# Optimization experiments

Measured on AMD Instinct MI355X. Metric: run time of the kernel, lower is better.

Reference implementation:

```python
import jax, jax.numpy as jnp
import numpy as np

B, D, E, H = 2048, 1024, 16, 4096
NUM_ACTIVE = 2
LN_EPS = 1e-5
NORM_EPS = 1e-12


def setup_inputs() -> dict:
    key = jax.random.key(0)
    ks = jax.random.split(key, 4)
    s1 = 1.0 / np.sqrt(D)
    s2 = 1.0 / np.sqrt(H)
    return {
        "input": jax.random.normal(ks[0], (B, D), jnp.float32),
        "ln_gamma": jnp.ones((D,), jnp.float32),
        "ln_beta": jnp.zeros((D,), jnp.float32),
        "expert_keys": jax.random.normal(ks[1], (D, E), jnp.float32),
        "W1": jax.random.normal(ks[2], (E, D, H), jnp.float32) * s1,
        "b1": jnp.zeros((E, H), jnp.float32),
        "W2": jax.random.normal(ks[3], (E, H, D), jnp.float32) * s2,
        "b2": jnp.zeros((E, D), jnp.float32),
    }


def reference(input, ln_gamma, ln_beta, expert_keys, W1, b1, W2, b2):
    # Gating: LayerNorm(input) @ normalize(expert_keys, dim=-1)
    mu = jnp.mean(input, axis=-1, keepdims=True)
    var = jnp.mean((input - mu) ** 2, axis=-1, keepdims=True)
    xn = (input - mu) / jnp.sqrt(var + LN_EPS) * ln_gamma + ln_beta
    # F.normalize(expert_keys, dim=-1): each row (per feature) normalized over experts
    keys = expert_keys / jnp.clip(
        jnp.linalg.norm(expert_keys, axis=-1, keepdims=True), NORM_EPS)
    logits = xn @ keys  # [B, E]
    # Top-k routing (argsort descending, take first num_active)
    top_vals, top_ids = jax.lax.top_k(logits, NUM_ACTIVE)  # [B, k]
    gates_k = jax.nn.softmax(top_vals, axis=-1)            # softmax over chosen logits
    gates = jnp.zeros_like(logits).at[
        jnp.arange(logits.shape[0])[:, None], top_ids].set(gates_k)  # [B, E]
    # Experts applied to RAW input (not the normalized gating input), dense-all-experts
    h = jax.nn.relu(jnp.einsum('bd,edh->beh', input, W1) + b1)   # [B, E, H]
    eo = jnp.einsum('beh,ehd->bed', h, W2) + b2                  # [B, E, D]
    # Weighted combine: only top-k experts have nonzero gates
    out = jnp.einsum('bed,be->bd', eo, gates)                    # [B, D]
    return out
```

## Files before the change

### kernel.cpp

```cpp
#include <hip/hip_runtime.h>
#include <hip/hip_bf16.h>
#include <cstdint>
#include <cstddef>

#define D_ 1024
#define H_ 4096
#define E_ 16
#define B_ 2048

constexpr int CAP = 384;

typedef __attribute__((ext_vector_type(4))) float f32x4;
typedef __attribute__((ext_vector_type(8))) short bf16x8;

__device__ __forceinline__ unsigned pack2(float a, float b) {
  __hip_bfloat162 h = __float22bfloat162_rn(make_float2(a, b));
  union { __hip_bfloat162 h2; unsigned u; } cv; cv.h2 = h;
  return cv.u;
}
__device__ __forceinline__ float bflo(unsigned u) { return __uint_as_float(u << 16); }
__device__ __forceinline__ float bfhi(unsigned u) { return __uint_as_float(u & 0xffff0000u); }

#define GLL16(g, l)                                                         \
  __builtin_amdgcn_global_load_lds(                                         \
      (const __attribute__((address_space(1))) void*)(g),                   \
      (__attribute__((address_space(3))) void*)(l), 16, 0, 0)

#define WAITV(n) asm volatile("s_waitcnt vmcnt(" #n ")" ::: "memory")
#define WAITL()  asm volatile("s_waitcnt lgkmcnt(0)" ::: "memory")
#define MEMBAR() asm volatile("" ::: "memory")
#define BAR() __builtin_amdgcn_s_barrier()

__global__ void moe_zero(int* __restrict__ cnt) {
  if (threadIdx.x < E_) cnt[threadIdx.x] = 0;
}

__global__ __launch_bounds__(256) void moe_gating3(
    const float* __restrict__ x, const float* __restrict__ gamma,
    const float* __restrict__ beta, const float* __restrict__ keys,
    int* __restrict__ cnt, int4* __restrict__ rmi, float2* __restrict__ rmg,
    unsigned short* __restrict__ xg)
{
  const int b = blockIdx.x, t = threadIdx.x;
  const int w = t >> 6;
  const float4 xv = ((const float4*)(x + (size_t)b * D_))[t];
  float s  = xv.x + xv.y + xv.z + xv.w;
  float sq = xv.x*xv.x + xv.y*xv.y + xv.z*xv.z + xv.w*xv.w;
#pragma unroll
  for (int off = 32; off >= 1; off >>= 1) {
    s  += __shfl_down(s, off);
    sq += __shfl_down(sq, off);
  }
  __shared__ float ssum[4], ssq[4], sstat[2];
  if ((t & 63) == 0) { ssum[w] = s; ssq[w] = sq; }
  __syncthreads();
  if (t == 0) {
    float S = ssum[0] + ssum[1] + ssum[2] + ssum[3];
    float Q = ssq[0] + ssq[1] + ssq[2] + ssq[3];
    float mu  = S * (1.0f / D_);
    float var = Q * (1.0f / D_) - mu * mu;
    sstat[0] = mu; sstat[1] = rsqrtf(var + 1e-5f);
  }
  __syncthreads();
  const float mu = sstat[0], rstd = sstat[1];
  const float4 gv = ((const float4*)gamma)[t];
  const float4 bv = ((const float4*)beta)[t];
  float xn[4] = {(xv.x-mu)*rstd*gv.x+bv.x, (xv.y-mu)*rstd*gv.y+bv.y,
                 (xv.z-mu)*rstd*gv.z+bv.z, (xv.w-mu)*rstd*gv.w+bv.w};
  float acc[E_];
#pragma unroll
  for (int e2 = 0; e2 < E_; ++e2) acc[e2] = 0.f;
#pragma unroll
  for (int j = 0; j < 4; ++j) {
    const int d = 4*t + j;
    const float* kr = keys + (size_t)d * E_;
    float kv[E_];
#pragma unroll
    for (int e2 = 0; e2 < E_; ++e2) kv[e2] = kr[e2];
    float nq = 0.f;
#pragma unroll
    for (int e2 = 0; e2 < E_; ++e2) nq += kv[e2] * kv[e2];
    const float sc = xn[j] / fmaxf(sqrtf(nq), 1e-12f);
#pragma unroll
    for (int e2 = 0; e2 < E_; ++e2) acc[e2] += sc * kv[e2];
  }
#pragma unroll
  for (int off = 1; off < 64; off <<= 1) {
#pragma unroll
    for (int e2 = 0; e2 < E_; ++e2) acc[e2] += __shfl_xor(acc[e2], off);
  }
  __shared__ float wred[4][E_];
  if ((t & 63) == 0) {
#pragma unroll
    for (int e2 = 0; e2 < E_; ++e2) wred[w][e2] = acc[e2];
  }
  __syncthreads();
  __shared__ int sE[2], sP[2];
  if (t == 0) {
    float lg[E_];
#pragma unroll
    for (int e2 = 0; e2 < E_; ++e2)
      lg[e2] = wred[0][e2] + wred[1][e2] + wred[2][e2] + wred[3][e2];
    float v0 = -1e30f; int e0 = 0;
    for (int e2 = 0; e2 < E_; ++e2) { if (lg[e2] > v0) { v0 = lg[e2]; e0 = e2; } }
    float v1 = -1e30f; int e1 = 0;
    for (int e2 = 0; e2 < E_; ++e2) { if (e2 == e0) continue; if (lg[e2] > v1) { v1 = lg[e2]; e1 = e2; } }
    const float g0 = 1.f / (1.f + __expf(v1 - v0));
    const float g1 = 1.f - g0;
    int p0 = atomicAdd(cnt + e0, 1); if (p0 >= CAP) p0 = CAP - 1;
    int p1 = atomicAdd(cnt + e1, 1); if (p1 >= CAP) p1 = CAP - 1;
    rmi[b] = make_int4(e0, p0, e1, p1);
    rmg[b] = make_float2(g0, g1);
    sE[0] = e0; sP[0] = p0;
    sE[1] = e1; sP[1] = p1;
  }
  __syncthreads();
  const uint2 pk = make_uint2(pack2(xv.x, xv.y), pack2(xv.z, xv.w));
#pragma unroll
  for (int i = 0; i < 2; ++i)
    ((uint2*)(xg + ((size_t)sE[i] * CAP + sP[i]) * D_))[t] = pk;
}

template<int KROW, int KLEN, int WN, int SPLITK, bool RELU>
__global__ void __launch_bounds__(256, 3)
moe_gemm(const unsigned short* __restrict__ Asrc, const float* __restrict__ W,
         const float* __restrict__ bias, const int* __restrict__ cnt,
         unsigned short* __restrict__ d0, unsigned short* __restrict__ d1,
         unsigned short* __restrict__ d2, unsigned short* __restrict__ d3)
{
  constexpr int NPHASE = KLEN / 32;
  constexpr int NT = WN / 128;
  constexpr int MT = 3;

  const int bx = blockIdx.x;
  const int xcd = bx & 7;
  int slot = bx >> 3;
  const int mt = slot % MT; slot /= MT;
  const int nt = slot % NT; slot /= NT;
  const int eh = slot & 1;  slot >>= 1;
  const int part = slot;
  const int e  = (xcd << 1) | eh;
  const int nb = nt * 128;
  const int koff = part * KLEN;
  unsigned short* dst = (part == 0) ? d0 : (part == 1) ? d1 : (part == 2) ? d2 : d3;

  int cntE = cnt[e]; if (cntE > CAP) cntE = CAP;
  if (mt * 128 >= cntE) return;

  const int t = threadIdx.x, w = t >> 6, lane = t & 63;
  const int l15 = lane & 15, l4 = lane >> 4;

  __shared__ __align__(16) unsigned short As[2][128 * 32];
  __shared__ __align__(16) unsigned short Bs[2][128 * 32];

  asm volatile("s_waitcnt vmcnt(0) lgkmcnt(0)" ::: "memory");

  const unsigned short* Ae = Asrc + (size_t)e * CAP * KROW + (size_t)mt * 128 * KROW + koff;
  const float* We = W + (size_t)e * KROW * WN + (size_t)koff * WN + nb;

  const unsigned short *srcA0, *srcA1;
  {
    const int c0 = t,        r0 = c0 >> 2;
    const int c1 = t + 256,  r1 = c1 >> 2;
    srcA0 = Ae + (size_t)r0 * KROW + ((c0 & 3) ^ ((r0 >> 1) & 3)) * 8;
    srcA1 = Ae + (size_t)r1 * KROW + ((c1 & 3) ^ ((r1 >> 1) & 3)) * 8;
  }
  const int bn = t & 127, bkh = t >> 7;
  const float* srcB = We + (size_t)(bkh * 16) * WN + bn;
  const int bo0 = bn * 64 + (((bkh * 2 + 0) ^ ((bn >> 1) & 3)) << 4);
  const int bo1 = bn * 64 + (((bkh * 2 + 1) ^ ((bn >> 1) & 3)) << 4);

  float R0[16], R1[16];

#define ISSUE_A(p, BUF) do {                                                \
    const int ko_ = (p) * 32;                                               \
    GLL16(srcA0 + ko_, &As[BUF][(0 * 256 + w * 64) * 8]);                   \
    GLL16(srcA1 + ko_, &As[BUF][(1 * 256 + w * 64) * 8]);                   \
  } while (0)

#define ISSUE_B(p, Rv) do {                                                 \
    const float* bp_ = srcB + (size_t)(p) * 32 * WN;                        \
    _Pragma("unroll")                                                       \
    for (int j = 0; j < 16; ++j)                                            \
      Rv[j] = bp_[(size_t)j * WN];                                          \
  } while (0)

#define WRITE(Rv, BUF) do {                                                 \
    uint4 q0_, q1_;                                                         \
    q0_.x = pack2(Rv[0],  Rv[1]);  q0_.y = pack2(Rv[2],  Rv[3]);            \
    q0_.z = pack2(Rv[4],  Rv[5]);  q0_.w = pack2(Rv[6],  Rv[7]);            \
    q1_.x = pack2(Rv[8],  Rv[9]);  q1_.y = pack2(Rv[10], Rv[11]);           \
    q1_.z = pack2(Rv[12], Rv[13]); q1_.w = pack2(Rv[14], Rv[15]);           \
    *(uint4*)((char*)&Bs[BUF][0] + bo0) = q0_;                              \
    *(uint4*)((char*)&Bs[BUF][0] + bo1) = q1_;                              \
  } while (0)

  f32x4 acc[8][2];
#pragma unroll
  for (int rf = 0; rf < 8; ++rf) { acc[rf][0] = f32x4{0,0,0,0}; acc[rf][1] = f32x4{0,0,0,0}; }

  const int swA = (l15 >> 1) & 3;
  const int mrow0 = mt * 128;

#define COMP(BUF) do {                                                      \
    bf16x8 BB[2];                                                           \
    _Pragma("unroll")                                                       \
    for (int cf = 0; cf < 2; ++cf) {                                        \
      const int n_ = w * 32 + cf * 16 + l15;                                \
      BB[cf] = *(const bf16x8*)((const char*)&Bs[BUF][0]                    \
               + (n_ * 64 + ((l4 ^ ((n_ >> 1) & 3)) << 4)));                \
    }                                                                       \
    __builtin_amdgcn_s_setprio(1);                                          \
    _Pragma("unroll")                                                       \
    for (int rf = 0; rf < 8; ++rf) {                                        \
      if (mrow0 + rf * 16 < cntE) {                                         \
        const bf16x8 a = *(const bf16x8*)&As[BUF][((rf * 16 + l15) * 4 + (l4 ^ swA)) * 8]; \
        acc[rf][0] = __builtin_amdgcn_mfma_f32_16x16x32_bf16(a, BB[0], acc[rf][0], 0,0,0); \
        acc[rf][1] = __builtin_amdgcn_mfma_f32_16x16x32_bf16(a, BB[1], acc[rf][1], 0,0,0); \
      }                                                                     \
    }                                                                       \
    __builtin_amdgcn_s_setprio(0);                                          \
  } while (0)

  ISSUE_A(0, 0); MEMBAR();
  ISSUE_B(0, R0); MEMBAR();
  ISSUE_B(1, R1);
#pragma unroll 1
  for (int p = 0; p < NPHASE; p += 2) {
    if (p + 1 < NPHASE) { WAITV(16); } else { WAITV(0); }
    WRITE(R0, 0);
    if (p + 1 < NPHASE) { ISSUE_A(p + 1, 1); }
    MEMBAR();
    if (p + 2 < NPHASE) { ISSUE_B(p + 2, R0); }
    WAITL(); BAR();
    COMP(0);
    BAR();
    if (p + 1 < NPHASE) {
      if (p + 2 < NPHASE) { WAITV(16); } else { WAITV(0); }
      WRITE(R1, 1);
      if (p + 2 < NPHASE) { ISSUE_A(p + 2, 0); }
      MEMBAR();
      if (p + 3 < NPHASE) { ISSUE_B(p + 3, R1); }
      WAITL(); BAR();
      COMP(1);
      BAR();
    }
  }
#undef ISSUE_A
#undef ISSUE_B
#undef WRITE
#undef COMP

  unsigned short* dbase = dst + (size_t)e * CAP * WN + nb + w * 32;
#pragma unroll
  for (int rf = 0; rf < 8; ++rf) {
    if (mrow0 + rf * 16 >= cntE && rf > 0) continue;
#pragma unroll
    for (int cf = 0; cf < 2; ++cf) {
      float bv = 0.f;
      if constexpr (RELU) bv = bias[e * WN + nb + w * 32 + cf * 16 + l15];
#pragma unroll
      for (int r = 0; r < 4; ++r) {
        const int row = mrow0 + rf * 16 + l4 * 4 + r;
        float v = acc[rf][cf][r];
        if constexpr (RELU) v = fmaxf(v + bv, 0.f);
        const unsigned u01 = pack2(v, __shfl_xor(v, 1));
        const float uo = __shfl_xor(__uint_as_float(u01), 2);
        if ((l15 & 3) == 0)
          *(uint2*)(dbase + (size_t)row * WN + cf * 16 + l15) =
              make_uint2(u01, __float_as_uint(uo));
      }
    }
  }
}

__global__ __launch_bounds__(256) void moe_comb(
    const unsigned short* __restrict__ p0, const unsigned short* __restrict__ p1,
    const unsigned short* __restrict__ p2, const unsigned short* __restrict__ p3,
    const float* __restrict__ b2, const int4* __restrict__ rmi,
    const float2* __restrict__ rmg, float* __restrict__ out)
{
  const int b = blockIdx.x, t = threadIdx.x;
  const int4 m = rmi[b];
  const float2 g = rmg[b];
  const int c = t * 4;
  const size_t offA = ((size_t)m.x * CAP + m.y) * D_ + c;
  const size_t offB = ((size_t)m.z * CAP + m.w) * D_ + c;
  float a0, a1, a2, a3, c0, c1, c2, c3;
  {
    const uint2 ua = *(const uint2*)(p0 + offA);
    const uint2 ub = *(const uint2*)(p0 + offB);
    a0 = bflo(ua.x); a1 = bfhi(ua.x); a2 = bflo(ua.y); a3 = bfhi(ua.y);
    c0 = bflo(ub.x); c1 = bfhi(ub.x); c2 = bflo(ub.y); c3 = bfhi(ub.y);
  }
  const unsigned short* parts[3] = { p1, p2, p3 };
#pragma unroll
  for (int i = 0; i < 3; ++i) {
    if (parts[i] != nullptr) {
      const uint2 ua = *(const uint2*)(parts[i] + offA);
      const uint2 ub = *(const uint2*)(parts[i] + offB);
      a0 += bflo(ua.x); a1 += bfhi(ua.x); a2 += bflo(ua.y); a3 += bfhi(ua.y);
      c0 += bflo(ub.x); c1 += bfhi(ub.x); c2 += bflo(ub.y); c3 += bfhi(ub.y);
    }
  }
  const float4 b2a = *(const float4*)(b2 + (size_t)m.x * D_ + c);
  const float4 b2b = *(const float4*)(b2 + (size_t)m.z * D_ + c);
  float4 o;
  o.x = g.x * (a0 + b2a.x) + g.y * (c0 + b2b.x);
  o.y = g.x * (a1 + b2a.y) + g.y * (c1 + b2b.y);
  o.z = g.x * (a2 + b2a.z) + g.y * (c2 + b2b.z);
  o.w = g.x * (a3 + b2a.w) + g.y * (c3 + b2b.w);
  *(float4*)(out + (size_t)b * D_ + c) = o;
}

extern "C" void kernel_launch(void* const* d_in, const int* in_sizes, int n_in,
                              void* d_out, int out_size, void* d_ws, size_t ws_size,
                              hipStream_t stream) {
  const float* x     = (const float*)d_in[0];
  const float* gamma = (const float*)d_in[1];
  const float* beta  = (const float*)d_in[2];
  const float* keys  = (const float*)d_in[3];
  const float* W1    = (const float*)d_in[4];
  const float* b1    = (const float*)d_in[5];
  const float* W2    = (const float*)d_in[6];
  const float* b2    = (const float*)d_in[7];
  float* out = (float*)d_out;

  char* ws = (char*)d_ws;
  const size_t OFF_RMI = 256;
  const size_t OFF_RMG = OFF_RMI + (size_t)B_ * 16;
  const size_t OFF_XG  = OFF_RMG + (size_t)B_ * 8;
  const size_t EO_SZ   = (size_t)E_ * CAP * D_ * 2;
  const size_t OFF_HW  = OFF_XG + EO_SZ;
  const size_t HW_SZ   = (size_t)E_ * CAP * H_ * 2;
  const size_t OFF_EO1 = OFF_HW + HW_SZ;
  const size_t NEED2   = OFF_EO1 + EO_SZ;
  const size_t NEED4   = OFF_EO1 + 3 * EO_SZ;

  int*    cnt = (int*)ws;
  int4*   rmi = (int4*)(ws + OFF_RMI);
  float2* rmg = (float2*)(ws + OFF_RMG);
  unsigned short* xg  = (unsigned short*)(ws + OFF_XG);
  unsigned short* eo0 = xg;
  unsigned short* hws = (unsigned short*)(ws + OFF_HW);

  moe_zero<<<1, 64, 0, stream>>>(cnt);
  moe_gating3<<<B_, 256, 0, stream>>>(x, gamma, beta, keys, cnt, rmi, rmg, xg);

  moe_gemm<D_, D_, H_, 1, true><<<1536, 256, 0, stream>>>(
      xg, W1, b1, cnt, hws, nullptr, nullptr, nullptr);

  if (ws_size >= NEED4) {
    unsigned short* eo1 = (unsigned short*)(ws + OFF_EO1);
    unsigned short* eo2 = (unsigned short*)(ws + OFF_EO1 + EO_SZ);
    unsigned short* eo3 = (unsigned short*)(ws + OFF_EO1 + 2 * EO_SZ);
    moe_gemm<H_, H_ / 4, D_, 4, false><<<1536, 256, 0, stream>>>(
        hws, W2, nullptr, cnt, eo0, eo1, eo2, eo3);
    moe_comb<<<B_, 256, 0, stream>>>(eo0, eo1, eo2, eo3, b2, rmi, rmg, out);
  } else if (ws_size >= NEED2) {
    unsigned short* eo1 = (unsigned short*)(ws + OFF_EO1);
    moe_gemm<H_, H_ / 2, D_, 2, false><<<768, 256, 0, stream>>>(
        hws, W2, nullptr, cnt, eo0, eo1, nullptr, nullptr);
    moe_comb<<<B_, 256, 0, stream>>>(eo0, eo1, nullptr, nullptr, b2, rmi, rmg, out);
  } else {
    moe_gemm<H_, H_, D_, 1, false><<<384, 256, 0, stream>>>(
        hws, W2, nullptr, cnt, eo0, nullptr, nullptr, nullptr);
    moe_comb<<<B_, 256, 0, stream>>>(eo0, nullptr, nullptr, nullptr, b2, rmi, rmg, out);
  }
}
```

Measured before the change: 297.0 us.

## Enlarge MoE GEMM tiles to 256 rows with 512-thread blocks and capacity 512

The grouped expert GEMM now uses 256x128 tiles computed by 8 waves, each owning 32 rows by all 128 columns, instead of 128x128 tiles split by column. Each fp32 weight tile converted to bf16 is therefore reused across twice as many token rows, which cuts the repeated weight loads and conversions. Expert capacity rises from 384 to 512, and the grid is re-decomposed into two M-tiles per expert. The costs are more padded work for experts with fewer tokens, more LDS per block and lower occupancy, and larger workspace buffers.

```diff
diff --git a/kernel.cpp b/kernel.cpp
--- a/kernel.cpp
+++ b/kernel.cpp
@@ -8,7 +8,7 @@
 #define E_ 16
 #define B_ 2048
 
-constexpr int CAP = 384;
+constexpr int CAP = 512;
 
 typedef __attribute__((ext_vector_type(4))) float f32x4;
 typedef __attribute__((ext_vector_type(8))) short bf16x8;
@@ -122,7 +122,7 @@
 }
 
 template<int KROW, int KLEN, int WN, int SPLITK, bool RELU>
-__global__ void __launch_bounds__(256, 3)
+__global__ void __launch_bounds__(512, 2)
 moe_gemm(const unsigned short* __restrict__ Asrc, const float* __restrict__ W,
          const float* __restrict__ bias, const int* __restrict__ cnt,
          unsigned short* __restrict__ d0, unsigned short* __restrict__ d1,
@@ -130,12 +130,11 @@
 {
   constexpr int NPHASE = KLEN / 32;
   constexpr int NT = WN / 128;
-  constexpr int MT = 3;
 
   const int bx = blockIdx.x;
   const int xcd = bx & 7;
   int slot = bx >> 3;
-  const int mt = slot % MT; slot /= MT;
+  const int mt = slot & 1;  slot >>= 1;
   const int nt = slot % NT; slot /= NT;
   const int eh = slot & 1;  slot >>= 1;
   const int part = slot;
@@ -145,78 +144,75 @@
   unsigned short* dst = (part == 0) ? d0 : (part == 1) ? d1 : (part == 2) ? d2 : d3;
 
   int cntE = cnt[e]; if (cntE > CAP) cntE = CAP;
-  if (mt * 128 >= cntE) return;
+  if (mt * 256 >= cntE) return;
 
   const int t = threadIdx.x, w = t >> 6, lane = t & 63;
   const int l15 = lane & 15, l4 = lane >> 4;
 
-  __shared__ __align__(16) unsigned short As[2][128 * 32];
+  __shared__ __align__(16) unsigned short As[2][256 * 32];
   __shared__ __align__(16) unsigned short Bs[2][128 * 32];
 
   asm volatile("s_waitcnt vmcnt(0) lgkmcnt(0)" ::: "memory");
 
-  const unsigned short* Ae = Asrc + (size_t)e * CAP * KROW + (size_t)mt * 128 * KROW + koff;
+  const unsigned short* Ae = Asrc + (size_t)e * CAP * KROW + (size_t)mt * 256 * KROW + koff;
   const float* We = W + (size_t)e * KROW * WN + (size_t)koff * WN + nb;
 
   const unsigned short *srcA0, *srcA1;
   {
     const int c0 = t,        r0 = c0 >> 2;
-    const int c1 = t + 256,  r1 = c1 >> 2;
+    const int c1 = t + 512,  r1 = c1 >> 2;
     srcA0 = Ae + (size_t)r0 * KROW + ((c0 & 3) ^ ((r0 >> 1) & 3)) * 8;
     srcA1 = Ae + (size_t)r1 * KROW + ((c1 & 3) ^ ((r1 >> 1) & 3)) * 8;
   }
-  const int bn = t & 127, bkh = t >> 7;
-  const float* srcB = We + (size_t)(bkh * 16) * WN + bn;
-  const int bo0 = bn * 64 + (((bkh * 2 + 0) ^ ((bn >> 1) & 3)) << 4);
-  const int bo1 = bn * 64 + (((bkh * 2 + 1) ^ ((bn >> 1) & 3)) << 4);
-
-  float R0[16], R1[16];
+  const int bn = t & 127, bkq = t >> 7;
+  const float* srcB = We + (size_t)(bkq * 8) * WN + bn;
+  const int bo = bn * 64 + ((bkq ^ ((bn >> 1) & 3)) << 4);
+
+  float R0[8], R1[8];
 
 #define ISSUE_A(p, BUF) do {                                                \
     const int ko_ = (p) * 32;                                               \
-    GLL16(srcA0 + ko_, &As[BUF][(0 * 256 + w * 64) * 8]);                   \
-    GLL16(srcA1 + ko_, &As[BUF][(1 * 256 + w * 64) * 8]);                   \
+    GLL16(srcA0 + ko_, &As[BUF][(0 * 512 + w * 64) * 8]);                   \
+    GLL16(srcA1 + ko_, &As[BUF][(1 * 512 + w * 64) * 8]);                   \
   } while (0)
 
 #define ISSUE_B(p, Rv) do {                                                 \
     const float* bp_ = srcB + (size_t)(p) * 32 * WN;                        \
     _Pragma("unroll")                                                       \
-    for (int j = 0; j < 16; ++j)                                            \
+    for (int j = 0; j < 8; ++j)                                             \
       Rv[j] = bp_[(size_t)j * WN];                                          \
   } while (0)
 
 #define WRITE(Rv, BUF) do {                                                 \
-    uint4 q0_, q1_;                                                         \
-    q0_.x = pack2(Rv[0],  Rv[1]);  q0_.y = pack2(Rv[2],  Rv[3]);            \
-    q0_.z = pack2(Rv[4],  Rv[5]);  q0_.w = pack2(Rv[6],  Rv[7]);            \
-    q1_.x = pack2(Rv[8],  Rv[9]);  q1_.y = pack2(Rv[10], Rv[11]);           \
-    q1_.z = pack2(Rv[12], Rv[13]); q1_.w = pack2(Rv[14], Rv[15]);           \
-    *(uint4*)((char*)&Bs[BUF][0] + bo0) = q0_;                              \
-    *(uint4*)((char*)&Bs[BUF][0] + bo1) = q1_;                              \
+    uint4 q_;                                                               \
+    q_.x = pack2(Rv[0], Rv[1]);  q_.y = pack2(Rv[2], Rv[3]);                \
+    q_.z = pack2(Rv[4], Rv[5]);  q_.w = pack2(Rv[6], Rv[7]);                \
+    *(uint4*)((char*)&Bs[BUF][0] + bo) = q_;                                \
   } while (0)
 
-  f32x4 acc[8][2];
-#pragma unroll
-  for (int rf = 0; rf < 8; ++rf) { acc[rf][0] = f32x4{0,0,0,0}; acc[rf][1] = f32x4{0,0,0,0}; }
+  f32x4 acc[2][8];
+#pragma unroll
+  for (int rf = 0; rf < 2; ++rf)
+#pragma unroll
+    for (int cf = 0; cf < 8; ++cf) acc[rf][cf] = f32x4{0,0,0,0};
 
   const int swA = (l15 >> 1) & 3;
-  const int mrow0 = mt * 128;
+  const int mrow0 = mt * 256;
+  const int wrow = w * 32;
 
 #define COMP(BUF) do {                                                      \
-    bf16x8 BB[2];                                                           \
-    _Pragma("unroll")                                                       \
-    for (int cf = 0; cf < 2; ++cf) {                                        \
-      const int n_ = w * 32 + cf * 16 + l15;                                \
-      BB[cf] = *(const bf16x8*)((const char*)&Bs[BUF][0]                    \
-               + (n_ * 64 + ((l4 ^ ((n_ >> 1) & 3)) << 4)));                \
-    }                                                                       \
     __builtin_amdgcn_s_setprio(1);                                          \
     _Pragma("unroll")                                                       \
-    for (int rf = 0; rf < 8; ++rf) {                                        \
-      if (mrow0 + rf * 16 < cntE) {                                         \
-        const bf16x8 a = *(const bf16x8*)&As[BUF][((rf * 16 + l15) * 4 + (l4 ^ swA)) * 8]; \
-        acc[rf][0] = __builtin_amdgcn_mfma_f32_16x16x32_bf16(a, BB[0], acc[rf][0], 0,0,0); \
-        acc[rf][1] = __builtin_amdgcn_mfma_f32_16x16x32_bf16(a, BB[1], acc[rf][1], 0,0,0); \
+    for (int cf = 0; cf < 8; ++cf) {                                        \
+      const int n_ = cf * 16 + l15;                                         \
+      const bf16x8 bb = *(const bf16x8*)((const char*)&Bs[BUF][0]           \
+               + (n_ * 64 + ((l4 ^ ((n_ >> 1) & 3)) << 4)));                \
+      _Pragma("unroll")                                                     \
+      for (int rf = 0; rf < 2; ++rf) {                                      \
+        if (mrow0 + wrow + rf * 16 < cntE) {                                \
+          const bf16x8 a = *(const bf16x8*)&As[BUF][((wrow + rf * 16 + l15) * 4 + (l4 ^ swA)) * 8]; \
+          acc[rf][cf] = __builtin_amdgcn_mfma_f32_16x16x32_bf16(a, bb, acc[rf][cf], 0,0,0); \
+        }                                                                   \
       }                                                                     \
     }                                                                       \
     __builtin_amdgcn_s_setprio(0);                                          \
@@ -227,7 +223,7 @@
   ISSUE_B(1, R1);
 #pragma unroll 1
   for (int p = 0; p < NPHASE; p += 2) {
-    if (p + 1 < NPHASE) { WAITV(16); } else { WAITV(0); }
+    if (p + 1 < NPHASE) { WAITV(8); } else { WAITV(0); }
     WRITE(R0, 0);
     if (p + 1 < NPHASE) { ISSUE_A(p + 1, 1); }
     MEMBAR();
@@ -236,7 +232,7 @@
     COMP(0);
     BAR();
     if (p + 1 < NPHASE) {
-      if (p + 2 < NPHASE) { WAITV(16); } else { WAITV(0); }
+      if (p + 2 < NPHASE) { WAITV(8); } else { WAITV(0); }
       WRITE(R1, 1);
       if (p + 2 < NPHASE) { ISSUE_A(p + 2, 0); }
       MEMBAR();
@@ -251,17 +247,17 @@
 #undef WRITE
 #undef COMP
 
-  unsigned short* dbase = dst + (size_t)e * CAP * WN + nb + w * 32;
-#pragma unroll
-  for (int rf = 0; rf < 8; ++rf) {
-    if (mrow0 + rf * 16 >= cntE && rf > 0) continue;
-#pragma unroll
-    for (int cf = 0; cf < 2; ++cf) {
+  unsigned short* dbase = dst + (size_t)e * CAP * WN + nb;
+#pragma unroll
+  for (int rf = 0; rf < 2; ++rf) {
+    if (mrow0 + wrow + rf * 16 >= cntE) continue;
+#pragma unroll
+    for (int cf = 0; cf < 8; ++cf) {
       float bv = 0.f;
-      if constexpr (RELU) bv = bias[e * WN + nb + w * 32 + cf * 16 + l15];
+      if constexpr (RELU) bv = bias[e * WN + nb + cf * 16 + l15];
 #pragma unroll
       for (int r = 0; r < 4; ++r) {
-        const int row = mrow0 + rf * 16 + l4 * 4 + r;
+        const int row = mrow0 + wrow + rf * 16 + l4 * 4 + r;
         float v = acc[rf][cf][r];
         if constexpr (RELU) v = fmaxf(v + bv, 0.f);
         const unsigned u01 = pack2(v, __shfl_xor(v, 1));
@@ -347,23 +343,23 @@
   moe_zero<<<1, 64, 0, stream>>>(cnt);
   moe_gating3<<<B_, 256, 0, stream>>>(x, gamma, beta, keys, cnt, rmi, rmg, xg);
 
-  moe_gemm<D_, D_, H_, 1, true><<<1536, 256, 0, stream>>>(
+  moe_gemm<D_, D_, H_, 1, true><<<1024, 512, 0, stream>>>(
       xg, W1, b1, cnt, hws, nullptr, nullptr, nullptr);
 
   if (ws_size >= NEED4) {
     unsigned short* eo1 = (unsigned short*)(ws + OFF_EO1);
     unsigned short* eo2 = (unsigned short*)(ws + OFF_EO1 + EO_SZ);
     unsigned short* eo3 = (unsigned short*)(ws + OFF_EO1 + 2 * EO_SZ);
-    moe_gemm<H_, H_ / 4, D_, 4, false><<<1536, 256, 0, stream>>>(
+    moe_gemm<H_, H_ / 4, D_, 4, false><<<1024, 512, 0, stream>>>(
         hws, W2, nullptr, cnt, eo0, eo1, eo2, eo3);
     moe_comb<<<B_, 256, 0, stream>>>(eo0, eo1, eo2, eo3, b2, rmi, rmg, out);
   } else if (ws_size >= NEED2) {
     unsigned short* eo1 = (unsigned short*)(ws + OFF_EO1);
-    moe_gemm<H_, H_ / 2, D_, 2, false><<<768, 256, 0, stream>>>(
+    moe_gemm<H_, H_ / 2, D_, 2, false><<<512, 512, 0, stream>>>(
         hws, W2, nullptr, cnt, eo0, eo1, nullptr, nullptr);
     moe_comb<<<B_, 256, 0, stream>>>(eo0, eo1, nullptr, nullptr, b2, rmi, rmg, out);
   } else {
-    moe_gemm<H_, H_, D_, 1, false><<<384, 256, 0, stream>>>(
+    moe_gemm<H_, H_, D_, 1, false><<<256, 512, 0, stream>>>(
         hws, W2, nullptr, cnt, eo0, nullptr, nullptr, nullptr);
     moe_comb<<<B_, 256, 0, stream>>>(eo0, nullptr, nullptr, nullptr, b2, rmi, rmg, out);
   }
```

New measurement: 318.8 us. +7.4%, slower.
